# Kernel tuning notes

Hardware: AMD Instinct MI355X
Metric: run time of the kernel (lower is better)

The kernel has to match this reference:

```python
import jax, jax.numpy as jnp
import numpy as np

N_DIST, H, W, K = 256, 256, 192, 129
DR, DR0, DELTA = 0.2, 0.2, 1e-11


def _dual_exp(d, b1, b2, b3, b4):
    return b1 * np.exp(-b2 * d) + b3 * np.exp(-b4 * d)


def setup_inputs() -> dict:
    key = jax.random.key(0)
    d = (np.arange(N_DIST) + 1.0) * DR                      # distances (cm)
    gaus_amp = _dual_exp(d, 1.0, 0.01, 0.1, 0.001)
    gaus_sig = 0.05 * d + 1.0
    bkg_amp = _dual_exp(d, 0.05, 0.05, 0.01, 0.005)
    bkg_sig = 0.08 * d + 2.0
    xk = np.arange(-(K // 2), K // 2 + 1) * DR / DR0        # (K,) kernel coords
    # gaussian kernel (get_gaus_layer)
    kernel_g = np.sqrt(gaus_amp)[:, None] * np.exp(-xk[None, :] ** 2 / (2 * gaus_sig[:, None] ** 2 + DELTA))
    # background kernels (get_bkg_layers) with emulated splines
    w_f = lambda t: np.exp(-np.abs(t))
    iso_f = lambda t: 1.0 / (1.0 + t ** 2)
    xw = xk[None, :] / bkg_sig[:, None]
    kernel_w = bkg_amp[:, None] * (DR / DR0) * w_f(xw)
    kernel_iso = bkg_amp[:, None] * (DR / DR0) * iso_f(xw)
    # normalization factor (configure)
    xs = np.linspace(-5.0, 5.0, 2001)
    Iw = np.trapz(w_f(xs), xs)
    Iiso = np.trapz(iso_f(xs), xs)
    Nw = 3 * bkg_amp * Iw * bkg_sig
    Niso = bkg_amp * Iiso * bkg_sig
    Ng2 = gaus_amp * 2 * np.pi * gaus_sig ** 2 * (DR0 / DR) ** 2
    norm = (Nw + Niso ** 2 + 1.0) * Ng2
    x = jax.random.uniform(key, (1, N_DIST, H, W), dtype=jnp.float32)
    return {
        "x": x,
        "kernel_g": jnp.asarray(kernel_g, jnp.float32),
        "kernel_w": jnp.asarray(kernel_w, jnp.float32),
        "kernel_iso": jnp.asarray(kernel_iso, jnp.float32),
        "norm": jnp.asarray(norm, jnp.float32),
    }


def _dwconv(x, kern, axis):
    """Depthwise 'same' Conv1d along `axis` of (N,H,W); channels = dim 0."""
    n = x.shape[0]
    perm = (2, 0, 1) if axis == 1 else (1, 0, 2)   # -> (batch, channels=N, length)
    inv = (1, 2, 0) if axis == 1 else (1, 0, 2)
    xb = jnp.transpose(x, perm)
    y = jax.lax.conv_general_dilated(
        xb, kern[:, None, :], (1,), 'SAME',
        feature_group_count=n, dimension_numbers=('NCH', 'OIH', 'NCH'))
    return jnp.transpose(y, inv)


def _rotate(x, ang):
    """Bilinear rotation of (N,S,S) in dims (1,2), zero padding (grid_sample-like)."""
    s = x.shape[1]
    c = (s - 1) * 0.5
    ca, sa = jnp.cos(ang), jnp.sin(ang)
    idx = jnp.arange(s, dtype=x.dtype) - c
    yy, xx = jnp.meshgrid(idx, idx, indexing='ij')
    sy = ca * yy + sa * xx + c   # inverse-rotated source coords
    sx = -sa * yy + ca * xx + c
    y0 = jnp.floor(sy)
    x0 = jnp.floor(sx)
    fy, fx = sy - y0, sx - x0
    y0i, x0i = y0.astype(jnp.int32), x0.astype(jnp.int32)

    def gat(yi, xi):
        valid = (yi >= 0) & (yi < s) & (xi >= 0) & (xi < s)
        v = x[:, jnp.clip(yi, 0, s - 1), jnp.clip(xi, 0, s - 1)]
        return jnp.where(valid, v, 0.0)

    return (gat(y0i, x0i) * (1 - fy) * (1 - fx)
            + gat(y0i, x0i + 1) * (1 - fy) * fx
            + gat(y0i + 1, x0i) * fy * (1 - fx)
            + gat(y0i + 1, x0i + 1) * fy * fx)


def reference(x, kernel_g, kernel_w, kernel_iso, norm):
    out = x[0]                                   # (N, H, W)
    out = _dwconv(out, kernel_g, 1)
    out = _dwconv(out, kernel_g, 2)
    iso = _dwconv(out, kernel_iso, 1)
    iso = _dwconv(iso, kernel_iso, 2)
    n, h, w = out.shape
    pad = (n - w) // 2
    padded = jnp.pad(out, ((0, 0), (0, 0), (pad, pad)))  # (N, H, H) square plane
    tails = jnp.zeros_like(padded)
    for i in range(3):                            # 0, 60, 120 degrees
        ang = float(np.deg2rad(60 * i))
        t = _rotate(padded, ang)
        t = _dwconv(t, kernel_w, 2)
        tails = tails + _rotate(t, -ang)
    tails = tails[:, :, pad:pad + w]
    out = (out + tails + iso) / norm[:, None, None]
    return out[None]
```

## Files before the change

### kernel.cpp

```cpp
#include <hip/hip_runtime.h>
#include <cmath>

#define CN   256
#define HN   256
#define WN   192
#define KN   129
#define RN   64
#define SN   256
#define PADN 32

#define BBR 92
#define BBP 96

template <int WD, bool ACC>
__global__ __launch_bounds__(256, 5) void conv_w_lds(const float* __restrict__ in,
                                                     const float* __restrict__ kern,
                                                     float* __restrict__ out) {
    constexpr int PITCH = 97;
    __shared__ float lds[64 * PITCH + 132];
    float* __restrict__ ldsK = lds + 64 * PITCH;
    const int tid = threadIdx.x;
    const int x0  = blockIdx.x * 64;
    const int h0  = blockIdx.y * 64;
    const int c   = blockIdx.z;
    const float* __restrict__ in_c = in + ((size_t)c * HN + h0) * WD;

    if (tid < 132) ldsK[tid] = (tid < KN) ? kern[c * KN + tid] : 0.f;

    const int wv = tid >> 6;
    const int l  = tid & 63;
    const int base  = l * PITCH + wv * 16;
    const int col32 = tid & 31;
    const int r8    = tid >> 5;

    float acc[16];
#pragma unroll
    for (int t = 0; t < 16; ++t) acc[t] = 0.f;

#pragma unroll 1
    for (int s = 0; s < 4; ++s) {
        __syncthreads();
        const int off = x0 + 32 * s - 64;
        if (off >= 0 && off + 96 <= WD) {
#pragma unroll
            for (int m = 0; m < 3; ++m)
#pragma unroll
                for (int k = 0; k < 8; ++k)
                    lds[(r8 + 8 * k) * PITCH + col32 + 32 * m] =
                        in_c[(size_t)(r8 + 8 * k) * WD + off + col32 + 32 * m];
        } else {
#pragma unroll
            for (int m = 0; m < 3; ++m)
#pragma unroll
                for (int k = 0; k < 8; ++k) {
                    int g  = off + col32 + 32 * m;
                    int gc = min(max(g, 0), WD - 1);
                    float v = in_c[(size_t)(r8 + 8 * k) * WD + gc];
                    lds[(r8 + 8 * k) * PITCH + col32 + 32 * m] = (g == gc) ? v : 0.f;
                }
        }
        __syncthreads();

        float H0[16], H1[16], H2[16];
#pragma unroll
        for (int i = 0; i < 16; ++i) H0[i] = lds[base + i];
#pragma unroll
        for (int i = 0; i < 16; ++i) H1[i] = lds[base + 16 + i];

        const float4* __restrict__ k4 = (const float4*)ldsK;
        float4 kc = k4[8 * s];
#pragma unroll
        for (int q = 0; q < 8; ++q) {
            float4 kn = (q < 7) ? k4[8 * s + q + 1] : kc;
#pragma unroll
            for (int u = 0; u < 4; ++u) {
                const int up = 4 * q + u;
                const float kj = (u == 0) ? kc.x : (u == 1) ? kc.y
                               : (u == 2) ? kc.z : kc.w;
#pragma unroll
                for (int t = 0; t < 16; ++t) {
                    const int e = up + t;
                    const float val = (e < 16) ? H0[e]
                                    : (e < 32) ? H1[e - 16] : H2[e - 32];
                    acc[t] = fmaf(val, kj, acc[t]);
                }
            }
            if (q == 0) {
#pragma unroll
                for (int i = 0; i < 16; ++i) H2[i] = lds[base + 32 + i];
            }
            kc = kn;
        }
        if (s == 3) {
            const float k128 = ldsK[128];
#pragma unroll
            for (int t = 0; t < 16; ++t) acc[t] = fmaf(H2[t], k128, acc[t]);
        }
    }

    float4* __restrict__ o4 =
        (float4*)(out + ((size_t)c * HN + h0 + l) * WD + x0 + wv * 16);
#pragma unroll
    for (int q = 0; q < 4; ++q) {
        float4 v;
        v.x = acc[4*q]; v.y = acc[4*q+1]; v.z = acc[4*q+2]; v.w = acc[4*q+3];
        if (ACC) {
            float4 o = o4[q];
            v.x += o.x; v.y += o.y; v.z += o.z; v.w += o.w;
        }
        o4[q] = v;
    }
}

__global__ __launch_bounds__(256, 5) void conv_h_lds(const float* __restrict__ in,
                                                     const float* __restrict__ kern,
                                                     float* __restrict__ out) {
    __shared__ float lds[96 * 64 + 132];
    float* __restrict__ ldsK = lds + 96 * 64;
    const int tid = threadIdx.x;
    const int x0  = blockIdx.x * 64;
    const int h0  = blockIdx.y * 64;
    const int c   = blockIdx.z;
    const float* __restrict__ in_c = in + (size_t)c * HN * WN + x0;

    if (tid < 132) ldsK[tid] = (tid < KN) ? kern[c * KN + tid] : 0.f;

    const int wv = tid >> 6;
    const int l  = tid & 63;
    const int baseRow = wv * 16;
    const int col = tid & 63;
    const int r4  = tid >> 6;

    float acc[16];
#pragma unroll
    for (int t = 0; t < 16; ++t) acc[t] = 0.f;

#pragma unroll 1
    for (int s = 0; s < 4; ++s) {
        __syncthreads();
        const int off = h0 + 32 * s - 64;
        if (off >= 0 && off + 96 <= HN) {
#pragma unroll
            for (int k = 0; k < 24; ++k)
                lds[(r4 + 4 * k) * 64 + col] =
                    in_c[(size_t)(off + r4 + 4 * k) * WN + col];
        } else {
#pragma unroll
            for (int k = 0; k < 24; ++k) {
                int g  = off + r4 + 4 * k;
                int gc = min(max(g, 0), HN - 1);
                float v = in_c[(size_t)gc * WN + col];
                lds[(r4 + 4 * k) * 64 + col] = (g == gc) ? v : 0.f;
            }
        }
        __syncthreads();

        float H0[16], H1[16], H2[16];
#pragma unroll
        for (int i = 0; i < 16; ++i) H0[i] = lds[(baseRow + i) * 64 + l];
#pragma unroll
        for (int i = 0; i < 16; ++i) H1[i] = lds[(baseRow + 16 + i) * 64 + l];

        const float4* __restrict__ k4 = (const float4*)ldsK;
        float4 kc = k4[8 * s];
#pragma unroll
        for (int q = 0; q < 8; ++q) {
            float4 kn = (q < 7) ? k4[8 * s + q + 1] : kc;
#pragma unroll
            for (int u = 0; u < 4; ++u) {
                const int up = 4 * q + u;
                const float kj = (u == 0) ? kc.x : (u == 1) ? kc.y
                               : (u == 2) ? kc.z : kc.w;
#pragma unroll
                for (int t = 0; t < 16; ++t) {
                    const int e = up + t;
                    const float val = (e < 16) ? H0[e]
                                    : (e < 32) ? H1[e - 16] : H2[e - 32];
                    acc[t] = fmaf(val, kj, acc[t]);
                }
            }
            if (q == 0) {
#pragma unroll
                for (int i = 0; i < 16; ++i)
                    H2[i] = lds[(baseRow + 32 + i) * 64 + l];
            }
            kc = kn;
        }
        if (s == 3) {
            const float k128 = ldsK[128];
#pragma unroll
            for (int t = 0; t < 16; ++t) acc[t] = fmaf(H2[t], k128, acc[t]);
        }
    }

    float* __restrict__ ob = out + ((size_t)c * HN + h0 + wv * 16) * WN + x0 + l;
#pragma unroll
    for (int t = 0; t < 16; ++t) ob[(size_t)t * WN] = acc[t];
}

__global__ __launch_bounds__(256) void rot_fwd_lds(const float* __restrict__ Cin,
                                                   float* __restrict__ out,
                                                   float ca, float sa) {
    __shared__ float tile[BBR * BBP];
    const int j0 = blockIdx.x * 64;
    const int i0 = blockIdx.y * 64;
    const int c  = blockIdx.z;
    const float cc = (SN - 1) * 0.5f;
    const float yA = (float)i0 - cc, yB = (float)(i0 + 63) - cc;
    const float xA = (float)j0 - cc, xB = (float)(j0 + 63) - cc;
    const float syAA = ca * yA + sa * xA + cc, syAB = ca * yA + sa * xB + cc;
    const float syBA = ca * yB + sa * xA + cc, syBB = ca * yB + sa * xB + cc;
    const float sxAA = -sa * yA + ca * xA + cc, sxAB = -sa * yA + ca * xB + cc;
    const float sxBA = -sa * yB + ca * xA + cc, sxBB = -sa * yB + ca * xB + cc;
    const int ybase = (int)floorf(fminf(fminf(syAA, syAB), fminf(syBA, syBB))) - 1;
    const int xbase = (int)floorf(fminf(fminf(sxAA, sxAB), fminf(sxBA, sxBB))) - 1;

    const float* __restrict__ base = Cin + (size_t)c * HN * WN;
    for (int t = threadIdx.x; t < BBR * BBP; t += 256) {
        const int r  = t / BBP;
        const int q  = t - r * BBP;
        const int gy = ybase + r;
        const int gx = xbase + q - PADN;
        float v = 0.f;
        if ((unsigned)gy < (unsigned)HN && (unsigned)gx < (unsigned)WN)
            v = base[(size_t)gy * WN + gx];
        tile[t] = v;
    }
    __syncthreads();

    const int l  = threadIdx.x & 63;
    const int r0 = threadIdx.x >> 6;
    const int j  = j0 + l;
    const float xx = (float)j - cc;
    float* __restrict__ ocol = out + (size_t)c * SN * SN + j;
#pragma unroll
    for (int t = 0; t < 16; ++t) {
        const int i = i0 + r0 + 4 * t;
        const float yy = (float)i - cc;
        const float sy = ca * yy + sa * xx + cc;
        const float sx = -sa * yy + ca * xx + cc;
        const float y0f = floorf(sy), x0f = floorf(sx);
        const float fy = sy - y0f, fx = sx - x0f;
        const int ly = (int)y0f - ybase;
        const int lx = (int)x0f - xbase;
        const float* p = tile + ly * BBP + lx;
        const float v00 = p[0], v01 = p[1], v10 = p[BBP], v11 = p[BBP + 1];
        ocol[(size_t)i * SN] = (1.f - fy) * ((1.f - fx) * v00 + fx * v01)
                             + fy * ((1.f - fx) * v10 + fx * v11);
    }
}

template <bool FINAL>
__global__ __launch_bounds__(256) void rot_bwd_lds(const float* __restrict__ U,
                                                   float* __restrict__ dst,
                                                   const float* __restrict__ accIn,
                                                   const float* __restrict__ norm,
                                                   float ca, float sa) {
    __shared__ float tile[BBR * BBP];
    const int x0 = blockIdx.x * 64;
    const int i0 = blockIdx.y * 64;
    const int c  = blockIdx.z;
    const float cc = (SN - 1) * 0.5f;
    const float yA = (float)i0 - cc, yB = (float)(i0 + 63) - cc;
    const float xA = (float)(x0 + PADN) - cc, xB = (float)(x0 + PADN + 63) - cc;
    const float syAA = ca * yA + sa * xA + cc, syAB = ca * yA + sa * xB + cc;
    const float syBA = ca * yB + sa * xA + cc, syBB = ca * yB + sa * xB + cc;
    const float sxAA = -sa * yA + ca * xA + cc, sxAB = -sa * yA + ca * xB + cc;
    const float sxBA = -sa * yB + ca * xA + cc, sxBB = -sa * yB + ca * xB + cc;
    const int ybase = (int)floorf(fminf(fminf(syAA, syAB), fminf(syBA, syBB))) - 1;
    const int xbase = (int)floorf(fminf(fminf(sxAA, sxAB), fminf(sxBA, sxBB))) - 1;

    const float* __restrict__ base = U + (size_t)c * SN * SN;
    for (int t = threadIdx.x; t < BBR * BBP; t += 256) {
        const int r  = t / BBP;
        const int q  = t - r * BBP;
        const int gy = ybase + r;
        const int gx = xbase + q;
        float v = 0.f;
        if ((unsigned)gy < (unsigned)SN && (unsigned)gx < (unsigned)SN)
            v = base[(size_t)gy * SN + gx];
        tile[t] = v;
    }
    __syncthreads();

    const int l  = threadIdx.x & 63;
    const int r0 = threadIdx.x >> 6;
    const int xc = x0 + l;
    const float xx = (float)(xc + PADN) - cc;
    float inv = 0.f;
    if constexpr (FINAL) inv = 1.f / norm[c];
#pragma unroll
    for (int t = 0; t < 16; ++t) {
        const int i = i0 + r0 + 4 * t;
        const float yy = (float)i - cc;
        const float sy = ca * yy + sa * xx + cc;
        const float sx = -sa * yy + ca * xx + cc;
        const float y0f = floorf(sy), x0f = floorf(sx);
        const float fy = sy - y0f, fx = sx - x0f;
        const int ly = (int)y0f - ybase;
        const int lx = (int)x0f - xbase;
        const float* p = tile + ly * BBP + lx;
        const float v00 = p[0], v01 = p[1], v10 = p[BBP], v11 = p[BBP + 1];
        const float val = (1.f - fy) * ((1.f - fx) * v00 + fx * v01)
                        + fy * ((1.f - fx) * v10 + fx * v11);
        const size_t idx = ((size_t)c * HN + i) * WN + xc;
        if constexpr (FINAL) {
            dst[idx] = (dst[idx] + accIn[idx] + val) * inv;
        } else {
            dst[idx] += val;
        }
    }
}

extern "C" void kernel_launch(void* const* d_in, const int* in_sizes, int n_in,
                              void* d_out, int out_size, void* d_ws, size_t ws_size,
                              hipStream_t stream) {
    const float* x    = (const float*)d_in[0];
    const float* kg   = (const float*)d_in[1];
    const float* kw   = (const float*)d_in[2];
    const float* kiso = (const float*)d_in[3];
    const float* norm = (const float*)d_in[4];

    float* C = (float*)d_out;
    float* ws = (float*)d_ws;
    const size_t IMG = (size_t)CN * HN * WN;
    const size_t PSQ = (size_t)CN * SN * SN;
    float* B   = ws;
    float* acc = ws + IMG;
    float* T   = ws + 2 * IMG;
    float* U   = T + PSQ;

    const dim3 blk256(256);
    const dim3 convHGrid(WN / 64, HN / 64, CN);
    const dim3 convW192Grid(WN / 64, HN / 64, CN);
    const dim3 convW256Grid(SN / 64, HN / 64, CN);
    const dim3 rotFGrid(SN / 64, SN / 64, CN);
    const dim3 rotBGrid(WN / 64, HN / 64, CN);

    conv_h_lds<<<convHGrid, blk256, 0, stream>>>(x, kg, B);
    conv_w_lds<WN, false><<<convW192Grid, blk256, 0, stream>>>(B, kg, C);
    conv_h_lds<<<convHGrid, blk256, 0, stream>>>(C, kiso, B);
    conv_w_lds<WN, false><<<convW192Grid, blk256, 0, stream>>>(B, kiso, acc);
    conv_w_lds<WN, true><<<convW192Grid, blk256, 0, stream>>>(C, kw, acc);
    const double a1 = 60.0 * M_PI / 180.0, a2 = 120.0 * M_PI / 180.0;
    const float c1 = (float)cos(a1), s1 = (float)sin(a1);
    const float c2 = (float)cos(a2), s2 = (float)sin(a2);

    rot_fwd_lds<<<rotFGrid, blk256, 0, stream>>>(C, T, c1, s1);
    conv_w_lds<SN, false><<<convW256Grid, blk256, 0, stream>>>(T, kw, U);
    rot_bwd_lds<false><<<rotBGrid, blk256, 0, stream>>>(U, acc, nullptr, nullptr, c1, -s1);

    rot_fwd_lds<<<rotFGrid, blk256, 0, stream>>>(C, T, c2, s2);
    conv_w_lds<SN, false><<<convW256Grid, blk256, 0, stream>>>(T, kw, U);
    rot_bwd_lds<true><<<rotBGrid, blk256, 0, stream>>>(U, C, acc, norm, c2, -s2);

    (void)in_sizes; (void)n_in; (void)out_size; (void)ws_size;
}
```

Baseline: 768.4 us.

## Load full conv halo once with 512-thread blocks and fewer outputs per thread

Both depthwise conv kernels now stage the whole 192-wide halo tile into LDS in a single pass with one barrier, replacing four staged loads with barriers in between. Blocks grow to 512 threads, and each thread computes 8 outputs instead of 16, which cuts register pressure and should raise occupancy. The W-conv result is transposed through LDS so global stores are coalesced. In exchange, LDS use per block roughly doubles, which may cap how many blocks fit per CU, and each thread does more LDS reads relative to its FMAs.

```diff
diff --git a/kernel.cpp b/kernel.cpp
--- a/kernel.cpp
+++ b/kernel.cpp
@@ -13,10 +13,10 @@
 #define BBP 96
 
 template <int WD, bool ACC>
-__global__ __launch_bounds__(256, 5) void conv_w_lds(const float* __restrict__ in,
+__global__ __launch_bounds__(512, 6) void conv_w_lds(const float* __restrict__ in,
                                                      const float* __restrict__ kern,
                                                      float* __restrict__ out) {
-    constexpr int PITCH = 97;
+    constexpr int PITCH = 193;
     __shared__ float lds[64 * PITCH + 132];
     float* __restrict__ ldsK = lds + 64 * PITCH;
     const int tid = threadIdx.x;
@@ -29,45 +29,48 @@
 
     const int wv = tid >> 6;
     const int l  = tid & 63;
-    const int base  = l * PITCH + wv * 16;
-    const int col32 = tid & 31;
-    const int r8    = tid >> 5;
-
-    float acc[16];
-#pragma unroll
-    for (int t = 0; t < 16; ++t) acc[t] = 0.f;
-
-#pragma unroll 1
+    const int base  = l * PITCH + wv * 8;
+    const int col64 = tid & 63;
+    const int r8    = tid >> 6;
+
+    const int off = x0 - 64;
+    if (off >= 0 && off + 192 <= WD) {
+#pragma unroll
+        for (int m = 0; m < 3; ++m)
+#pragma unroll
+            for (int k = 0; k < 8; ++k)
+                lds[(r8 + 8 * k) * PITCH + col64 + 64 * m] =
+                    in_c[(size_t)(r8 + 8 * k) * WD + off + col64 + 64 * m];
+    } else {
+#pragma unroll
+        for (int m = 0; m < 3; ++m)
+#pragma unroll
+            for (int k = 0; k < 8; ++k) {
+                int g  = off + col64 + 64 * m;
+                int gc = min(max(g, 0), WD - 1);
+                float v = in_c[(size_t)(r8 + 8 * k) * WD + gc];
+                lds[(r8 + 8 * k) * PITCH + col64 + 64 * m] = (g == gc) ? v : 0.f;
+            }
+    }
+    __syncthreads();
+
+    float acc[8];
+#pragma unroll
+    for (int t = 0; t < 8; ++t) acc[t] = 0.f;
+
+    float B0[8], B1[8], B2[8], B3[8], B4[8];
+    const float4* __restrict__ k4 = (const float4*)ldsK;
+#pragma unroll
     for (int s = 0; s < 4; ++s) {
-        __syncthreads();
-        const int off = x0 + 32 * s - 64;
-        if (off >= 0 && off + 96 <= WD) {
-#pragma unroll
-            for (int m = 0; m < 3; ++m)
-#pragma unroll
-                for (int k = 0; k < 8; ++k)
-                    lds[(r8 + 8 * k) * PITCH + col32 + 32 * m] =
-                        in_c[(size_t)(r8 + 8 * k) * WD + off + col32 + 32 * m];
-        } else {
-#pragma unroll
-            for (int m = 0; m < 3; ++m)
-#pragma unroll
-                for (int k = 0; k < 8; ++k) {
-                    int g  = off + col32 + 32 * m;
-                    int gc = min(max(g, 0), WD - 1);
-                    float v = in_c[(size_t)(r8 + 8 * k) * WD + gc];
-                    lds[(r8 + 8 * k) * PITCH + col32 + 32 * m] = (g == gc) ? v : 0.f;
-                }
-        }
-        __syncthreads();
-
-        float H0[16], H1[16], H2[16];
-#pragma unroll
-        for (int i = 0; i < 16; ++i) H0[i] = lds[base + i];
-#pragma unroll
-        for (int i = 0; i < 16; ++i) H1[i] = lds[base + 16 + i];
-
-        const float4* __restrict__ k4 = (const float4*)ldsK;
+        const int sb = base + 32 * s;
+#pragma unroll
+        for (int i = 0; i < 8; ++i) B0[i] = lds[sb + i];
+#pragma unroll
+        for (int i = 0; i < 8; ++i) B1[i] = lds[sb + 8 + i];
+#pragma unroll
+        for (int i = 0; i < 8; ++i) B2[i] = lds[sb + 16 + i];
+#pragma unroll
+        for (int i = 0; i < 8; ++i) B3[i] = lds[sb + 24 + i];
         float4 kc = k4[8 * s];
 #pragma unroll
         for (int q = 0; q < 8; ++q) {
@@ -78,45 +81,47 @@
                 const float kj = (u == 0) ? kc.x : (u == 1) ? kc.y
                                : (u == 2) ? kc.z : kc.w;
 #pragma unroll
-                for (int t = 0; t < 16; ++t) {
+                for (int t = 0; t < 8; ++t) {
                     const int e = up + t;
-                    const float val = (e < 16) ? H0[e]
-                                    : (e < 32) ? H1[e - 16] : H2[e - 32];
+                    const float val = (e < 8)  ? B0[e]
+                                    : (e < 16) ? B1[e - 8]
+                                    : (e < 24) ? B2[e - 16]
+                                    : (e < 32) ? B3[e - 24] : B4[e - 32];
                     acc[t] = fmaf(val, kj, acc[t]);
                 }
             }
             if (q == 0) {
 #pragma unroll
-                for (int i = 0; i < 16; ++i) H2[i] = lds[base + 32 + i];
+                for (int i = 0; i < 8; ++i) B4[i] = lds[sb + 32 + i];
             }
             kc = kn;
         }
         if (s == 3) {
             const float k128 = ldsK[128];
 #pragma unroll
-            for (int t = 0; t < 16; ++t) acc[t] = fmaf(H2[t], k128, acc[t]);
-        }
-    }
-
-    float4* __restrict__ o4 =
-        (float4*)(out + ((size_t)c * HN + h0 + l) * WD + x0 + wv * 16);
-#pragma unroll
-    for (int q = 0; q < 4; ++q) {
-        float4 v;
-        v.x = acc[4*q]; v.y = acc[4*q+1]; v.z = acc[4*q+2]; v.w = acc[4*q+3];
-        if (ACC) {
-            float4 o = o4[q];
-            v.x += o.x; v.y += o.y; v.z += o.z; v.w += o.w;
-        }
-        o4[q] = v;
-    }
-}
-
-__global__ __launch_bounds__(256, 5) void conv_h_lds(const float* __restrict__ in,
+            for (int t = 0; t < 8; ++t) acc[t] = fmaf(B4[t], k128, acc[t]);
+        }
+    }
+
+    __syncthreads();
+#pragma unroll
+    for (int i = 0; i < 8; ++i) lds[base + i] = acc[i];
+    __syncthreads();
+    float* __restrict__ ob = out + ((size_t)c * HN + h0) * WD + x0;
+#pragma unroll
+    for (int k = 0; k < 8; ++k) {
+        const int r = r8 + 8 * k;
+        float v = lds[r * PITCH + col64];
+        if (ACC) v += ob[(size_t)r * WD + col64];
+        ob[(size_t)r * WD + col64] = v;
+    }
+}
+
+__global__ __launch_bounds__(512, 6) void conv_h_lds(const float* __restrict__ in,
                                                      const float* __restrict__ kern,
                                                      float* __restrict__ out) {
-    __shared__ float lds[96 * 64 + 132];
-    float* __restrict__ ldsK = lds + 96 * 64;
+    __shared__ float lds[192 * 64 + 132];
+    float* __restrict__ ldsK = lds + 192 * 64;
     const int tid = threadIdx.x;
     const int x0  = blockIdx.x * 64;
     const int h0  = blockIdx.y * 64;
@@ -127,41 +132,44 @@
 
     const int wv = tid >> 6;
     const int l  = tid & 63;
-    const int baseRow = wv * 16;
+    const int baseRow = wv * 8;
     const int col = tid & 63;
-    const int r4  = tid >> 6;
-
-    float acc[16];
-#pragma unroll
-    for (int t = 0; t < 16; ++t) acc[t] = 0.f;
-
-#pragma unroll 1
+    const int r8  = tid >> 6;
+
+    const int off = h0 - 64;
+    if (off >= 0 && off + 192 <= HN) {
+#pragma unroll
+        for (int k = 0; k < 24; ++k)
+            lds[(r8 + 8 * k) * 64 + col] =
+                in_c[(size_t)(off + r8 + 8 * k) * WN + col];
+    } else {
+#pragma unroll
+        for (int k = 0; k < 24; ++k) {
+            int g  = off + r8 + 8 * k;
+            int gc = min(max(g, 0), HN - 1);
+            float v = in_c[(size_t)gc * WN + col];
+            lds[(r8 + 8 * k) * 64 + col] = (g == gc) ? v : 0.f;
+        }
+    }
+    __syncthreads();
+
+    float acc[8];
+#pragma unroll
+    for (int t = 0; t < 8; ++t) acc[t] = 0.f;
+
+    float B0[8], B1[8], B2[8], B3[8], B4[8];
+    const float4* __restrict__ k4 = (const float4*)ldsK;
+#pragma unroll
     for (int s = 0; s < 4; ++s) {
-        __syncthreads();
-        const int off = h0 + 32 * s - 64;
-        if (off >= 0 && off + 96 <= HN) {
-#pragma unroll
-            for (int k = 0; k < 24; ++k)
-                lds[(r4 + 4 * k) * 64 + col] =
-                    in_c[(size_t)(off + r4 + 4 * k) * WN + col];
-        } else {
-#pragma unroll
-            for (int k = 0; k < 24; ++k) {
-                int g  = off + r4 + 4 * k;
-                int gc = min(max(g, 0), HN - 1);
-                float v = in_c[(size_t)gc * WN + col];
-                lds[(r4 + 4 * k) * 64 + col] = (g == gc) ? v : 0.f;
-            }
-        }
-        __syncthreads();
-
-        float H0[16], H1[16], H2[16];
-#pragma unroll
-        for (int i = 0; i < 16; ++i) H0[i] = lds[(baseRow + i) * 64 + l];
-#pragma unroll
-        for (int i = 0; i < 16; ++i) H1[i] = lds[(baseRow + 16 + i) * 64 + l];
-
-        const float4* __restrict__ k4 = (const float4*)ldsK;
+        const int sr = baseRow + 32 * s;
+#pragma unroll
+        for (int i = 0; i < 8; ++i) B0[i] = lds[(sr + i) * 64 + l];
+#pragma unroll
+        for (int i = 0; i < 8; ++i) B1[i] = lds[(sr + 8 + i) * 64 + l];
+#pragma unroll
+        for (int i = 0; i < 8; ++i) B2[i] = lds[(sr + 16 + i) * 64 + l];
+#pragma unroll
+        for (int i = 0; i < 8; ++i) B3[i] = lds[(sr + 24 + i) * 64 + l];
         float4 kc = k4[8 * s];
 #pragma unroll
         for (int q = 0; q < 8; ++q) {
@@ -172,30 +180,31 @@
                 const float kj = (u == 0) ? kc.x : (u == 1) ? kc.y
                                : (u == 2) ? kc.z : kc.w;
 #pragma unroll
-                for (int t = 0; t < 16; ++t) {
+                for (int t = 0; t < 8; ++t) {
                     const int e = up + t;
-                    const float val = (e < 16) ? H0[e]
-                                    : (e < 32) ? H1[e - 16] : H2[e - 32];
+                    const float val = (e < 8)  ? B0[e]
+                                    : (e < 16) ? B1[e - 8]
+                                    : (e < 24) ? B2[e - 16]
+                                    : (e < 32) ? B3[e - 24] : B4[e - 32];
                     acc[t] = fmaf(val, kj, acc[t]);
                 }
             }
             if (q == 0) {
 #pragma unroll
-                for (int i = 0; i < 16; ++i)
-                    H2[i] = lds[(baseRow + 32 + i) * 64 + l];
+                for (int i = 0; i < 8; ++i) B4[i] = lds[(sr + 32 + i) * 64 + l];
             }
             kc = kn;
         }
         if (s == 3) {
             const float k128 = ldsK[128];
 #pragma unroll
-            for (int t = 0; t < 16; ++t) acc[t] = fmaf(H2[t], k128, acc[t]);
-        }
-    }
-
-    float* __restrict__ ob = out + ((size_t)c * HN + h0 + wv * 16) * WN + x0 + l;
-#pragma unroll
-    for (int t = 0; t < 16; ++t) ob[(size_t)t * WN] = acc[t];
+            for (int t = 0; t < 8; ++t) acc[t] = fmaf(B4[t], k128, acc[t]);
+        }
+    }
+
+    float* __restrict__ ob = out + ((size_t)c * HN + h0 + baseRow) * WN + x0 + l;
+#pragma unroll
+    for (int t = 0; t < 8; ++t) ob[(size_t)t * WN] = acc[t];
 }
 
 __global__ __launch_bounds__(256) void rot_fwd_lds(const float* __restrict__ Cin,
@@ -331,27 +340,28 @@
     float* U   = T + PSQ;
 
     const dim3 blk256(256);
+    const dim3 blk512(512);
     const dim3 convHGrid(WN / 64, HN / 64, CN);
     const dim3 convW192Grid(WN / 64, HN / 64, CN);
     const dim3 convW256Grid(SN / 64, HN / 64, CN);
     const dim3 rotFGrid(SN / 64, SN / 64, CN);
     const dim3 rotBGrid(WN / 64, HN / 64, CN);
 
-    conv_h_lds<<<convHGrid, blk256, 0, stream>>>(x, kg, B);
-    conv_w_lds<WN, false><<<convW192Grid, blk256, 0, stream>>>(B, kg, C);
-    conv_h_lds<<<convHGrid, blk256, 0, stream>>>(C, kiso, B);
-    conv_w_lds<WN, false><<<convW192Grid, blk256, 0, stream>>>(B, kiso, acc);
-    conv_w_lds<WN, true><<<convW192Grid, blk256, 0, stream>>>(C, kw, acc);
+    conv_h_lds<<<convHGrid, blk512, 0, stream>>>(x, kg, B);
+    conv_w_lds<WN, false><<<convW192Grid, blk512, 0, stream>>>(B, kg, C);
+    conv_h_lds<<<convHGrid, blk512, 0, stream>>>(C, kiso, B);
+    conv_w_lds<WN, false><<<convW192Grid, blk512, 0, stream>>>(B, kiso, acc);
+    conv_w_lds<WN, true><<<convW192Grid, blk512, 0, stream>>>(C, kw, acc);
     const double a1 = 60.0 * M_PI / 180.0, a2 = 120.0 * M_PI / 180.0;
     const float c1 = (float)cos(a1), s1 = (float)sin(a1);
     const float c2 = (float)cos(a2), s2 = (float)sin(a2);
 
     rot_fwd_lds<<<rotFGrid, blk256, 0, stream>>>(C, T, c1, s1);
-    conv_w_lds<SN, false><<<convW256Grid, blk256, 0, stream>>>(T, kw, U);
+    conv_w_lds<SN, false><<<convW256Grid, blk512, 0, stream>>>(T, kw, U);
     rot_bwd_lds<false><<<rotBGrid, blk256, 0, stream>>>(U, acc, nullptr, nullptr, c1, -s1);
 
     rot_fwd_lds<<<rotFGrid, blk256, 0, stream>>>(C, T, c2, s2);
-    conv_w_lds<SN, false><<<convW256Grid, blk256, 0, stream>>>(T, kw, U);
+    conv_w_lds<SN, false><<<convW256Grid, blk512, 0, stream>>>(T, kw, U);
     rot_bwd_lds<true><<<rotBGrid, blk256, 0, stream>>>(U, C, acc, norm, c2, -s2);
 
     (void)in_sizes; (void)n_in; (void)out_size; (void)ws_size;
```

Result: no change. 762.0 us (-0.8%).

## Enlarge conv tiles to cut halo reloads and stage whole rows in LDS

Applied to the files above, without the earlier changes.

The width convolution now loads one wide tile (96 or 128 output columns plus a 128-column halo) into LDS once per block of 512 threads, instead of reloading overlapping 96-wide slices in four stages. It then writes results back through LDS for coalesced stores. The height convolution now loads a full 256-row column strip per channel with float4 loads, and each thread computes 32 outputs using ping-pong register buffers. This is meant to reduce redundant global halo traffic and barriers, at the cost of more LDS and registers per block and possibly lower occupancy.

```diff
diff --git a/kernel.cpp b/kernel.cpp
--- a/kernel.cpp
+++ b/kernel.cpp
@@ -12,62 +12,71 @@
 #define BBR 92
 #define BBP 96
 
-template <int WD, bool ACC>
-__global__ __launch_bounds__(256, 5) void conv_w_lds(const float* __restrict__ in,
+template <int TW, int WD, bool ACC>
+__global__ __launch_bounds__(512, 4) void conv_w_lds(const float* __restrict__ in,
                                                      const float* __restrict__ kern,
                                                      float* __restrict__ out) {
-    constexpr int PITCH = 97;
+    constexpr int NO    = TW / 8;
+    constexpr int TWW   = TW + 128;
+    constexpr int PITCH = TWW + 1;
+    constexpr int NB    = (2 * NO + 31) / NO;
     __shared__ float lds[64 * PITCH + 132];
     float* __restrict__ ldsK = lds + 64 * PITCH;
     const int tid = threadIdx.x;
-    const int x0  = blockIdx.x * 64;
+    const int x0  = blockIdx.x * TW;
     const int h0  = blockIdx.y * 64;
     const int c   = blockIdx.z;
     const float* __restrict__ in_c = in + ((size_t)c * HN + h0) * WD;
 
     if (tid < 132) ldsK[tid] = (tid < KN) ? kern[c * KN + tid] : 0.f;
 
+    const int colg = tid & 63;
+    const int rr   = tid >> 6;
+    const int off  = x0 - 64;
+
+    if (off >= 0 && off + TWW <= WD) {
+#pragma unroll
+        for (int m = 0; m < 4; ++m) {
+            if (colg + 64 * m < TWW) {
+#pragma unroll
+                for (int k = 0; k < 8; ++k)
+                    lds[(rr + 8 * k) * PITCH + colg + 64 * m] =
+                        in_c[(size_t)(rr + 8 * k) * WD + off + colg + 64 * m];
+            }
+        }
+    } else {
+#pragma unroll
+        for (int m = 0; m < 4; ++m) {
+            if (colg + 64 * m < TWW) {
+#pragma unroll
+                for (int k = 0; k < 8; ++k) {
+                    int g  = off + colg + 64 * m;
+                    int gc = min(max(g, 0), WD - 1);
+                    float v = in_c[(size_t)(rr + 8 * k) * WD + gc];
+                    lds[(rr + 8 * k) * PITCH + colg + 64 * m] = (g == gc) ? v : 0.f;
+                }
+            }
+        }
+    }
+    __syncthreads();
+
     const int wv = tid >> 6;
     const int l  = tid & 63;
-    const int base  = l * PITCH + wv * 16;
-    const int col32 = tid & 31;
-    const int r8    = tid >> 5;
-
-    float acc[16];
-#pragma unroll
-    for (int t = 0; t < 16; ++t) acc[t] = 0.f;
-
-#pragma unroll 1
+    const int base = l * PITCH + wv * NO;
+
+    float acc[NO];
+#pragma unroll
+    for (int t = 0; t < NO; ++t) acc[t] = 0.f;
+
+    float H[4][NO];
+    const float4* __restrict__ k4 = (const float4*)ldsK;
+#pragma unroll
     for (int s = 0; s < 4; ++s) {
-        __syncthreads();
-        const int off = x0 + 32 * s - 64;
-        if (off >= 0 && off + 96 <= WD) {
-#pragma unroll
-            for (int m = 0; m < 3; ++m)
-#pragma unroll
-                for (int k = 0; k < 8; ++k)
-                    lds[(r8 + 8 * k) * PITCH + col32 + 32 * m] =
-                        in_c[(size_t)(r8 + 8 * k) * WD + off + col32 + 32 * m];
-        } else {
-#pragma unroll
-            for (int m = 0; m < 3; ++m)
-#pragma unroll
-                for (int k = 0; k < 8; ++k) {
-                    int g  = off + col32 + 32 * m;
-                    int gc = min(max(g, 0), WD - 1);
-                    float v = in_c[(size_t)(r8 + 8 * k) * WD + gc];
-                    lds[(r8 + 8 * k) * PITCH + col32 + 32 * m] = (g == gc) ? v : 0.f;
-                }
-        }
-        __syncthreads();
-
-        float H0[16], H1[16], H2[16];
-#pragma unroll
-        for (int i = 0; i < 16; ++i) H0[i] = lds[base + i];
-#pragma unroll
-        for (int i = 0; i < 16; ++i) H1[i] = lds[base + 16 + i];
-
-        const float4* __restrict__ k4 = (const float4*)ldsK;
+        const int sb = base + 32 * s;
+#pragma unroll
+        for (int k = 0; k < NB - 1; ++k)
+#pragma unroll
+            for (int i = 0; i < NO; ++i) H[k][i] = lds[sb + k * NO + i];
         float4 kc = k4[8 * s];
 #pragma unroll
         for (int q = 0; q < 8; ++q) {
@@ -78,124 +87,145 @@
                 const float kj = (u == 0) ? kc.x : (u == 1) ? kc.y
                                : (u == 2) ? kc.z : kc.w;
 #pragma unroll
-                for (int t = 0; t < 16; ++t) {
+                for (int t = 0; t < NO; ++t) {
                     const int e = up + t;
-                    const float val = (e < 16) ? H0[e]
-                                    : (e < 32) ? H1[e - 16] : H2[e - 32];
+                    const float val = (e < NO)     ? H[0][e]
+                                    : (e < 2 * NO) ? H[1][e - NO]
+                                    : (e < 3 * NO) ? H[2][e - 2 * NO]
+                                                   : H[3][e - 3 * NO];
                     acc[t] = fmaf(val, kj, acc[t]);
                 }
             }
             if (q == 0) {
 #pragma unroll
-                for (int i = 0; i < 16; ++i) H2[i] = lds[base + 32 + i];
+                for (int i = 0; i < NO; ++i)
+                    H[NB - 1][i] = lds[sb + (NB - 1) * NO + i];
             }
             kc = kn;
         }
         if (s == 3) {
             const float k128 = ldsK[128];
 #pragma unroll
-            for (int t = 0; t < 16; ++t) acc[t] = fmaf(H2[t], k128, acc[t]);
-        }
-    }
-
-    float4* __restrict__ o4 =
-        (float4*)(out + ((size_t)c * HN + h0 + l) * WD + x0 + wv * 16);
-#pragma unroll
-    for (int q = 0; q < 4; ++q) {
-        float4 v;
-        v.x = acc[4*q]; v.y = acc[4*q+1]; v.z = acc[4*q+2]; v.w = acc[4*q+3];
-        if (ACC) {
-            float4 o = o4[q];
-            v.x += o.x; v.y += o.y; v.z += o.z; v.w += o.w;
-        }
-        o4[q] = v;
-    }
-}
-
-__global__ __launch_bounds__(256, 5) void conv_h_lds(const float* __restrict__ in,
+            for (int t = 0; t < NO; ++t) {
+                const int e = 32 + t;
+                const float val = (e < NO)     ? H[0][e]
+                                : (e < 2 * NO) ? H[1][e - NO]
+                                : (e < 3 * NO) ? H[2][e - 2 * NO]
+                                               : H[3][e - 3 * NO];
+                acc[t] = fmaf(val, k128, acc[t]);
+            }
+        }
+    }
+
+    __syncthreads();
+#pragma unroll
+    for (int i = 0; i < NO; ++i) lds[base + i] = acc[i];
+    __syncthreads();
+    float* __restrict__ obase = out + ((size_t)c * HN + h0) * WD + x0;
+#pragma unroll
+    for (int k = 0; k < (64 * TW) / 512; ++k) {
+        const int idx = k * 512 + tid;
+        const int r  = idx / TW;
+        const int cl = idx - r * TW;
+        float v = lds[r * PITCH + cl];
+        if (ACC) v += obase[(size_t)r * WD + cl];
+        obase[(size_t)r * WD + cl] = v;
+    }
+}
+
+__global__ __launch_bounds__(512, 4) void conv_h_lds(const float* __restrict__ in,
                                                      const float* __restrict__ kern,
                                                      float* __restrict__ out) {
-    __shared__ float lds[96 * 64 + 132];
-    float* __restrict__ ldsK = lds + 96 * 64;
+    __shared__ float lds[256 * 64 + 132];
+    float* __restrict__ ldsK = lds + 256 * 64;
     const int tid = threadIdx.x;
     const int x0  = blockIdx.x * 64;
-    const int h0  = blockIdx.y * 64;
-    const int c   = blockIdx.z;
+    const int c   = blockIdx.y;
     const float* __restrict__ in_c = in + (size_t)c * HN * WN + x0;
 
     if (tid < 132) ldsK[tid] = (tid < KN) ? kern[c * KN + tid] : 0.f;
+
+    {
+        const int f4 = (tid & 15) * 4;
+        const int rw = tid >> 4;
+#pragma unroll
+        for (int p = 0; p < 8; ++p) {
+            const int r = rw + 32 * p;
+            *(float4*)(lds + r * 64 + f4) =
+                *(const float4*)(in_c + (size_t)r * WN + f4);
+        }
+    }
+    __syncthreads();
 
     const int wv = tid >> 6;
     const int l  = tid & 63;
-    const int baseRow = wv * 16;
-    const int col = tid & 63;
-    const int r4  = tid >> 6;
-
-    float acc[16];
-#pragma unroll
-    for (int t = 0; t < 16; ++t) acc[t] = 0.f;
-
-#pragma unroll 1
-    for (int s = 0; s < 4; ++s) {
-        __syncthreads();
-        const int off = h0 + 32 * s - 64;
-        if (off >= 0 && off + 96 <= HN) {
-#pragma unroll
-            for (int k = 0; k < 24; ++k)
-                lds[(r4 + 4 * k) * 64 + col] =
-                    in_c[(size_t)(off + r4 + 4 * k) * WN + col];
-        } else {
-#pragma unroll
-            for (int k = 0; k < 24; ++k) {
-                int g  = off + r4 + 4 * k;
-                int gc = min(max(g, 0), HN - 1);
-                float v = in_c[(size_t)gc * WN + col];
-                lds[(r4 + 4 * k) * 64 + col] = (g == gc) ? v : 0.f;
-            }
-        }
-        __syncthreads();
-
-        float H0[16], H1[16], H2[16];
-#pragma unroll
-        for (int i = 0; i < 16; ++i) H0[i] = lds[(baseRow + i) * 64 + l];
-#pragma unroll
-        for (int i = 0; i < 16; ++i) H1[i] = lds[(baseRow + 16 + i) * 64 + l];
-
-        const float4* __restrict__ k4 = (const float4*)ldsK;
-        float4 kc = k4[8 * s];
-#pragma unroll
-        for (int q = 0; q < 8; ++q) {
-            float4 kn = (q < 7) ? k4[8 * s + q + 1] : kc;
-#pragma unroll
-            for (int u = 0; u < 4; ++u) {
-                const int up = 4 * q + u;
-                const float kj = (u == 0) ? kc.x : (u == 1) ? kc.y
-                               : (u == 2) ? kc.z : kc.w;
-#pragma unroll
-                for (int t = 0; t < 16; ++t) {
-                    const int e = up + t;
-                    const float val = (e < 16) ? H0[e]
-                                    : (e < 32) ? H1[e - 16] : H2[e - 32];
-                    acc[t] = fmaf(val, kj, acc[t]);
-                }
-            }
-            if (q == 0) {
-#pragma unroll
-                for (int i = 0; i < 16; ++i)
-                    H2[i] = lds[(baseRow + 32 + i) * 64 + l];
-            }
-            kc = kn;
-        }
-        if (s == 3) {
-            const float k128 = ldsK[128];
-#pragma unroll
-            for (int t = 0; t < 16; ++t) acc[t] = fmaf(H2[t], k128, acc[t]);
-        }
-    }
-
-    float* __restrict__ ob = out + ((size_t)c * HN + h0 + wv * 16) * WN + x0 + l;
-#pragma unroll
-    for (int t = 0; t < 16; ++t) ob[(size_t)t * WN] = acc[t];
+    const int rbase = wv * 32 - 64;
+
+    float acc[32];
+#pragma unroll
+    for (int t = 0; t < 32; ++t) acc[t] = 0.f;
+
+    float B0[32], B1[32];
+
+#define RDBLK(BUF, rfirst)                                                    \
+    {                                                                         \
+        const int rf = (rfirst);                                              \
+        if (rf >= 0 && rf + 31 < HN) {                                        \
+            _Pragma("unroll")                                                 \
+            for (int i = 0; i < 32; ++i) BUF[i] = lds[(rf + i) * 64 + l];     \
+        } else {                                                              \
+            _Pragma("unroll")                                                 \
+            for (int i = 0; i < 32; ++i) {                                    \
+                const int r  = rf + i;                                        \
+                const int rc = min(max(r, 0), HN - 1);                        \
+                const float v = lds[rc * 64 + l];                             \
+                BUF[i] = (r == rc) ? v : 0.f;                                 \
+            }                                                                 \
+        }                                                                     \
+    }
+
+#define STAGE(s, LOW, HIGH)                                                   \
+    {                                                                         \
+        const float4* __restrict__ k4 = (const float4*)ldsK;                  \
+        float4 kc = k4[8 * (s)];                                              \
+        _Pragma("unroll")                                                     \
+        for (int q = 0; q < 8; ++q) {                                         \
+            float4 kn = (q < 7) ? k4[8 * (s) + q + 1] : kc;                   \
+            _Pragma("unroll")                                                 \
+            for (int u = 0; u < 4; ++u) {                                     \
+                const float kj = (u == 0) ? kc.x : (u == 1) ? kc.y            \
+                               : (u == 2) ? kc.z : kc.w;                      \
+                _Pragma("unroll")                                             \
+                for (int t = 0; t < 32; ++t) {                                \
+                    const int e = 4 * q + u + t;                              \
+                    const float val = (e < 32) ? LOW[e] : HIGH[e - 32];       \
+                    acc[t] = fmaf(val, kj, acc[t]);                           \
+                }                                                             \
+            }                                                                 \
+            kc = kn;                                                          \
+        }                                                                     \
+    }
+
+    RDBLK(B0, rbase);
+    RDBLK(B1, rbase + 32);
+    STAGE(0, B0, B1);
+    RDBLK(B0, rbase + 64);
+    STAGE(1, B1, B0);
+    RDBLK(B1, rbase + 96);
+    STAGE(2, B0, B1);
+    RDBLK(B0, rbase + 128);
+    STAGE(3, B1, B0);
+    {
+        const float k128 = ldsK[128];
+#pragma unroll
+        for (int t = 0; t < 32; ++t) acc[t] = fmaf(B0[t], k128, acc[t]);
+    }
+#undef RDBLK
+#undef STAGE
+
+    float* __restrict__ ob = out + ((size_t)c * HN + wv * 32) * WN + x0 + l;
+#pragma unroll
+    for (int t = 0; t < 32; ++t) ob[(size_t)t * WN] = acc[t];
 }
 
 __global__ __launch_bounds__(256) void rot_fwd_lds(const float* __restrict__ Cin,
@@ -331,27 +361,28 @@
     float* U   = T + PSQ;
 
     const dim3 blk256(256);
-    const dim3 convHGrid(WN / 64, HN / 64, CN);
-    const dim3 convW192Grid(WN / 64, HN / 64, CN);
-    const dim3 convW256Grid(SN / 64, HN / 64, CN);
+    const dim3 blk512(512);
+    const dim3 convHGrid(WN / 64, CN);
+    const dim3 convW192Grid(2, HN / 64, CN);
+    const dim3 convW256Grid(2, HN / 64, CN);
     const dim3 rotFGrid(SN / 64, SN / 64, CN);
     const dim3 rotBGrid(WN / 64, HN / 64, CN);
 
-    conv_h_lds<<<convHGrid, blk256, 0, stream>>>(x, kg, B);
-    conv_w_lds<WN, false><<<convW192Grid, blk256, 0, stream>>>(B, kg, C);
-    conv_h_lds<<<convHGrid, blk256, 0, stream>>>(C, kiso, B);
-    conv_w_lds<WN, false><<<convW192Grid, blk256, 0, stream>>>(B, kiso, acc);
-    conv_w_lds<WN, true><<<convW192Grid, blk256, 0, stream>>>(C, kw, acc);
+    conv_h_lds<<<convHGrid, blk512, 0, stream>>>(x, kg, B);
+    conv_w_lds<96, WN, false><<<convW192Grid, blk512, 0, stream>>>(B, kg, C);
+    conv_h_lds<<<convHGrid, blk512, 0, stream>>>(C, kiso, B);
+    conv_w_lds<96, WN, false><<<convW192Grid, blk512, 0, stream>>>(B, kiso, acc);
+    conv_w_lds<96, WN, true><<<convW192Grid, blk512, 0, stream>>>(C, kw, acc);
     const double a1 = 60.0 * M_PI / 180.0, a2 = 120.0 * M_PI / 180.0;
     const float c1 = (float)cos(a1), s1 = (float)sin(a1);
     const float c2 = (float)cos(a2), s2 = (float)sin(a2);
 
     rot_fwd_lds<<<rotFGrid, blk256, 0, stream>>>(C, T, c1, s1);
-    conv_w_lds<SN, false><<<convW256Grid, blk256, 0, stream>>>(T, kw, U);
+    conv_w_lds<128, SN, false><<<convW256Grid, blk512, 0, stream>>>(T, kw, U);
     rot_bwd_lds<false><<<rotBGrid, blk256, 0, stream>>>(U, acc, nullptr, nullptr, c1, -s1);
 
     rot_fwd_lds<<<rotFGrid, blk256, 0, stream>>>(C, T, c2, s2);
-    conv_w_lds<SN, false><<<convW256Grid, blk256, 0, stream>>>(T, kw, U);
+    conv_w_lds<128, SN, false><<<convW256Grid, blk512, 0, stream>>>(T, kw, U);
     rot_bwd_lds<true><<<rotBGrid, blk256, 0, stream>>>(U, C, acc, norm, c2, -s2);
 
     (void)in_sizes; (void)n_in; (void)out_size; (void)ws_size;
```

After: 865.1 us. +12.6%, slower.
